# Performance work log

Hardware: AMD Instinct MI355X
Metric: run time of the kernel (lower is better)

## Reference

```python
import jax, jax.numpy as jnp
import numpy as np

C = 128  # out_channels per head for every layer
LAYERS = [(8, 4), (512, 2), (256, 1)]  # (in_dim, heads)
PARAM_NAMES = [f"{n}{l}" for l in (1, 2, 3)
               for n in ("Wl", "bl", "Wr", "br", "We", "att", "bo", "lnw", "lnb")]
N_NODES, N_EDGES, N_GRAPHS = 50000, 800000, 64


def _gatv2(x, src, dst, ea, Wl, bl, Wr, br, We, att, bo, H, N):
    # PyG GATv2Conv (share_weights=False, concat=True, negative_slope=0.2)
    xl = (x @ Wl + bl).reshape(N, H, C)          # lin_l -> source transform
    xr = (x @ Wr + br).reshape(N, H, C)          # lin_r -> dest transform
    ee = (ea @ We).reshape(-1, H, C)             # lin_edge (no bias)
    s = jax.nn.leaky_relu(xl[src] + xr[dst] + ee, 0.2)  # [E,H,C]
    logit = jnp.einsum('ehc,hc->eh', s, att)     # per-edge attention logits
    # segment softmax over incoming edges of each destination node
    m = jax.ops.segment_max(logit, dst, num_segments=N)
    a = jnp.exp(logit - m[dst])
    a = a / (jax.ops.segment_sum(a, dst, num_segments=N)[dst] + 1e-16)
    out = jax.ops.segment_sum(xl[src] * a[:, :, None], dst, num_segments=N)
    return out.reshape(N, H * C) + bo


def _graph_layernorm(x, w, b):
    # PyG LayerNorm(mode='graph') called without batch: normalize over ALL
    # nodes and features jointly, then per-feature affine.
    mu = x.mean()
    sd = x.std()
    return (x - mu) / (sd + 1e-5) * w + b


def _forward(x, edge_index, edge_attr, batch, params):
    N = x.shape[0]
    src, dst = edge_index[0], edge_index[1]
    # add_self_loops with fill_value='mean': self-loop edge_attr = mean of
    # attrs of edges entering that node (0 if none)
    cnt = jax.ops.segment_sum(jnp.ones((src.shape[0],), x.dtype), dst, num_segments=N)
    loop_attr = jax.ops.segment_sum(edge_attr, dst, num_segments=N) / jnp.maximum(cnt, 1.0)[:, None]
    ar = jnp.arange(N, dtype=src.dtype)
    src2 = jnp.concatenate([src, ar])
    dst2 = jnp.concatenate([dst, ar])
    ea2 = jnp.concatenate([edge_attr, loop_attr], axis=0)

    h = x
    for l, (_, H) in enumerate(LAYERS, 1):
        p = lambda n: params[f"{n}{l}"]
        h = _gatv2(h, src2, dst2, ea2, p("Wl"), p("bl"), p("Wr"), p("br"),
                   p("We"), p("att"), p("bo"), H, N)
        h = jax.nn.elu(_graph_layernorm(h, p("lnw"), p("lnb")))
        # dropout(0.25) is identity in eval mode

    # global mean pool || global max pool
    gcnt = jax.ops.segment_sum(jnp.ones((N,), h.dtype), batch, num_segments=N_GRAPHS)
    mean = jax.ops.segment_sum(h, batch, num_segments=N_GRAPHS) / jnp.maximum(gcnt, 1.0)[:, None]
    mx = jax.ops.segment_max(h, batch, num_segments=N_GRAPHS)
    mx = jnp.where(jnp.isfinite(mx), mx, 0.0)
    return jnp.concatenate([mean, mx], axis=1)  # [G, 256]


def setup_inputs() -> dict:
    key = jax.random.key(0)
    ks = iter(jax.random.split(key, 64))
    x = jax.random.normal(next(ks), (N_NODES, 8), jnp.float32)
    edge_index = jax.random.randint(next(ks), (2, N_EDGES), 0, N_NODES, dtype=jnp.int32)
    edge_attr = jax.random.normal(next(ks), (N_EDGES, 3), jnp.float32)
    batch = jnp.sort(jax.random.randint(next(ks), (N_NODES,), 0, N_GRAPHS, dtype=jnp.int32))

    def lin(k, i, o):
        return jax.random.normal(k, (i, o), jnp.float32) * np.float32(1.0 / np.sqrt(i))

    params = {}
    for l, (din, H) in enumerate(LAYERS, 1):
        params[f"Wl{l}"] = lin(next(ks), din, H * C)
        params[f"bl{l}"] = jnp.zeros((H * C,), jnp.float32)
        params[f"Wr{l}"] = lin(next(ks), din, H * C)
        params[f"br{l}"] = jnp.zeros((H * C,), jnp.float32)
        params[f"We{l}"] = lin(next(ks), 3, H * C)
        params[f"att{l}"] = jax.random.normal(next(ks), (H, C), jnp.float32) * np.float32(0.1)
        params[f"bo{l}"] = jnp.zeros((H * C,), jnp.float32)
        params[f"lnw{l}"] = jnp.ones((H * C,), jnp.float32)
        params[f"lnb{l}"] = jnp.zeros((H * C,), jnp.float32)
    return {"x": x, "edge_index": edge_index, "edge_attr": edge_attr, "batch": batch, **params}


def reference(x, edge_index, edge_attr, batch,
              Wl1, bl1, Wr1, br1, We1, att1, bo1, lnw1, lnb1,
              Wl2, bl2, Wr2, br2, We2, att2, bo2, lnw2, lnb2,
              Wl3, bl3, Wr3, br3, We3, att3, bo3, lnw3, lnb3):
    vals = [Wl1, bl1, Wr1, br1, We1, att1, bo1, lnw1, lnb1,
            Wl2, bl2, Wr2, br2, We2, att2, bo2, lnw2, lnb2,
            Wl3, bl3, Wr3, br3, We3, att3, bo3, lnw3, lnb3]
    return _forward(x, edge_index, edge_attr, batch, dict(zip(PARAM_NAMES, vals)))
```

## Files before the change

### kernel.cpp

```cpp
#include <hip/hip_runtime.h>
#include <hip/hip_bf16.h>
#include <math.h>

#define N_NODES 50000
#define N_EDGES 800000
#define N_GRAPHS 64
#define E2_TOTAL (N_EDGES + N_NODES)

typedef unsigned short u16;
typedef __attribute__((ext_vector_type(8))) short s16x8;
typedef __attribute__((ext_vector_type(4))) float f32x4;
typedef __attribute__((ext_vector_type(2))) float f32x2;

__device__ __forceinline__ u16 f2bf(float f) {
    unsigned u = __float_as_uint(f);
    u += 0x7fffu + ((u >> 16) & 1u);
    return (u16)(u >> 16);
}
__device__ __forceinline__ void unpack2(unsigned v, float& a, float& b) {
    a = __uint_as_float(v << 16);
    b = __uint_as_float(v & 0xffff0000u);
}
__device__ __forceinline__ f32x2 up2(unsigned v) {
    f32x2 r;
    r.x = __uint_as_float(v << 16);
    r.y = __uint_as_float(v & 0xffff0000u);
    return r;
}
__device__ __forceinline__ unsigned pack2(float a, float b) {
    return (unsigned)f2bf(a) | ((unsigned)f2bf(b) << 16);
}
__device__ __forceinline__ float elu_fast(float u) {
    return u > 0.f ? u : __expf(u) - 1.f;
}


__global__ __launch_bounds__(256) void deg_kernel(const int* __restrict__ ei,
                                                  const float* __restrict__ eattr,
                                                  int* __restrict__ deg,
                                                  float* __restrict__ asum, int E) {
    int e = blockIdx.x * 256 + threadIdx.x;
    if (e >= E) return;
    int dst = ei[E + e];
    atomicAdd(&deg[dst], 1);
    atomicAdd(&asum[dst * 3 + 0], eattr[e * 3 + 0]);
    atomicAdd(&asum[dst * 3 + 1], eattr[e * 3 + 1]);
    atomicAdd(&asum[dst * 3 + 2], eattr[e * 3 + 2]);
}

__global__ __launch_bounds__(1024) void scan_kernel(const int* __restrict__ deg,
                                                    int* __restrict__ rowptr,
                                                    int* __restrict__ cursor, int N) {
    __shared__ int wsum[16];
    __shared__ int carry_s;
    int tid = threadIdx.x, lane = tid & 63, wid = tid >> 6;
    if (tid == 0) carry_s = 0;
    __syncthreads();
    for (int base = 0; base < N; base += 4096) {
        int i0 = base + tid * 4;
        int d0 = (i0 + 0 < N) ? deg[i0 + 0] + 1 : 0;
        int d1 = (i0 + 1 < N) ? deg[i0 + 1] + 1 : 0;
        int d2 = (i0 + 2 < N) ? deg[i0 + 2] + 1 : 0;
        int d3 = (i0 + 3 < N) ? deg[i0 + 3] + 1 : 0;
        int v = d0 + d1 + d2 + d3;
        int x = v;
        #pragma unroll
        for (int off = 1; off < 64; off <<= 1) {
            int t = __shfl_up(x, off);
            if (lane >= off) x += t;
        }
        if (lane == 63) wsum[wid] = x;
        __syncthreads();
        if (wid == 0) {
            int y = (lane < 16) ? wsum[lane] : 0;
            #pragma unroll
            for (int off = 1; off < 16; off <<= 1) {
                int t = __shfl_up(y, off);
                if (lane >= off) y += t;
            }
            if (lane < 16) wsum[lane] = y;
        }
        __syncthreads();
        int woff = (wid > 0) ? wsum[wid - 1] : 0;
        int excl = carry_s + woff + x - v;
        if (i0 + 0 < N) { rowptr[i0 + 0] = excl;                cursor[i0 + 0] = excl; }
        if (i0 + 1 < N) { rowptr[i0 + 1] = excl + d0;           cursor[i0 + 1] = excl + d0; }
        if (i0 + 2 < N) { rowptr[i0 + 2] = excl + d0 + d1;      cursor[i0 + 2] = excl + d0 + d1; }
        if (i0 + 3 < N) { rowptr[i0 + 3] = excl + d0 + d1 + d2; cursor[i0 + 3] = excl + d0 + d1 + d2; }
        __syncthreads();
        if (tid == 1023) carry_s += wsum[15];
        __syncthreads();
    }
    if (threadIdx.x == 0) rowptr[N] = carry_s;
}

__global__ __launch_bounds__(256) void fill_kernel(const int* __restrict__ ei,
                                                   const float* __restrict__ eattr,
                                                   const float* __restrict__ asum,
                                                   const int* __restrict__ deg,
                                                   int* __restrict__ cursor,
                                                   float4* __restrict__ meta,
                                                   int E, int E2) {
    int e = blockIdx.x * 256 + threadIdx.x;
    if (e >= E2) return;
    int src, dst;
    float a0, a1, a2;
    if (e < E) {
        src = ei[e]; dst = ei[E + e];
        a0 = eattr[(size_t)e * 3 + 0];
        a1 = eattr[(size_t)e * 3 + 1];
        a2 = eattr[(size_t)e * 3 + 2];
    } else {
        src = e - E; dst = src;
        float inv = 1.0f / (float)max(deg[dst], 1);
        a0 = asum[(size_t)dst * 3 + 0] * inv;
        a1 = asum[(size_t)dst * 3 + 1] * inv;
        a2 = asum[(size_t)dst * 3 + 2] * inv;
    }
    int pos = atomicAdd(&cursor[dst], 1);
    meta[pos] = make_float4(a0, a1, a2, __int_as_float(src));
}


__global__ __launch_bounds__(256) void xw8_dual(const float* __restrict__ x,
                                                const float* __restrict__ Wl,
                                                const float* __restrict__ bl,
                                                const float* __restrict__ Wr,
                                                const float* __restrict__ br,
                                                u16* __restrict__ Xa,
                                                u16* __restrict__ Xb, int N) {
    __shared__ float sWl[8 * 512], sWr[8 * 512];
    __shared__ float sbl[512], sbr[512];
    __shared__ float sx[64][8];
    int tid = threadIdx.x;
    int nb = blockIdx.x * 64;
    for (int i = tid; i < 8 * 512; i += 256) { sWl[i] = Wl[i]; sWr[i] = Wr[i]; }
    for (int i = tid; i < 512; i += 256) { sbl[i] = bl[i]; sbr[i] = br[i]; }
    for (int i = tid; i < 64 * 8; i += 256) {
        int j = i >> 3, k = i & 7;
        int n = nb + j;
        sx[j][k] = (n < N) ? x[(size_t)n * 8 + k] : 0.f;
    }
    __syncthreads();
    for (int it = 0; it < 64; it++) {
        int i = tid + it * 256;
        int j = i >> 8, c2 = (i & 255) * 2;
        int n = nb + j;
        if (n < N) {
            float l0 = sbl[c2], l1 = sbl[c2 + 1];
            float r0 = sbr[c2], r1 = sbr[c2 + 1];
            #pragma unroll
            for (int k = 0; k < 8; k++) {
                float xv = sx[j][k];
                l0 += xv * sWl[k * 512 + c2];
                l1 += xv * sWl[k * 512 + c2 + 1];
                r0 += xv * sWr[k * 512 + c2];
                r1 += xv * sWr[k * 512 + c2 + 1];
            }
            *reinterpret_cast<unsigned*>(Xa + (size_t)n * 512 + c2) = pack2(l0, l1);
            *reinterpret_cast<unsigned*>(Xb + (size_t)n * 512 + c2) = pack2(r0, r1);
        }
    }
}


__device__ __forceinline__ float2 reduce_buckets(const double* __restrict__ buck,
                                                 double count) {
    __shared__ float2 res;
    int t = threadIdx.x;
    double s  = buck[t * 2]     + buck[(t + 256) * 2];
    double s2 = buck[t * 2 + 1] + buck[(t + 256) * 2 + 1];
    #pragma unroll
    for (int off = 32; off; off >>= 1) {
        s += __shfl_xor(s, off);
        s2 += __shfl_xor(s2, off);
    }
    __shared__ double a[4], b[4];
    int wid = t >> 6, lane = t & 63;
    if (lane == 0) { a[wid] = s; b[wid] = s2; }
    __syncthreads();
    if (t == 0) {
        double S = a[0] + a[1] + a[2] + a[3];
        double S2 = b[0] + b[1] + b[2] + b[3];
        double mu = S / count;
        double var = S2 / count - mu * mu;
        float sd = (float)sqrt(var > 0.0 ? var : 0.0);
        res.x = (float)mu;
        res.y = 1.f / (sd + 1e-5f);
    }
    __syncthreads();
    return res;
}


__global__ __launch_bounds__(256) void wt_dual(const float* __restrict__ WL,
                                               const float* __restrict__ WR,
                                               u16* __restrict__ WtL,
                                               u16* __restrict__ WtR, int K, int M) {
    const float* W = blockIdx.z ? WR : WL;
    u16* Wt = blockIdx.z ? WtR : WtL;
    __shared__ u16 t[64][65];
    int kb = blockIdx.x * 64, mb = blockIdx.y * 64;
    int tid = threadIdx.x;
    for (int i = tid; i < 64 * 64; i += 256) {
        int k = i >> 6, m = i & 63;
        t[m][k] = f2bf(W[(size_t)(kb + k) * M + mb + m]);
    }
    __syncthreads();
    for (int i = tid; i < 64 * 64; i += 256) {
        int m = i >> 6, k = i & 63;
        Wt[(size_t)(mb + m) * K + kb + k] = t[m][k];
    }
}


__global__ __launch_bounds__(256) void gemm_dual(const u16* __restrict__ A,
                                                 const u16* __restrict__ BtL,
                                                 const u16* __restrict__ BtR,
                                                 const float* __restrict__ biasL,
                                                 const float* __restrict__ biasR,
                                                 u16* __restrict__ YL,
                                                 u16* __restrict__ YR,
                                                 const double* __restrict__ buck,
                                                 double count,
                                                 const float* __restrict__ lnw,
                                                 const float* __restrict__ lnb,
                                                 int N, int K, int M) {
    const u16* Bt = blockIdx.z ? BtR : BtL;
    const float* bias = blockIdx.z ? biasR : biasL;
    u16* Y = blockIdx.z ? YR : YL;
    constexpr int BM = 128, BK = 64;
    __shared__ u16 As[BM][BK];
    __shared__ u16 Bs[BM][BK];
    __shared__ float sLw[512], sLb[512];
    float2 lp = reduce_buckets(buck, count);
    float muf = lp.x, rs = lp.y;
    int tid = threadIdx.x;
    for (int i = tid; i < K; i += 256) { sLw[i] = lnw[i] * rs; sLb[i] = lnb[i]; }
    int wid = tid >> 6, lane = tid & 63;
    int wm = (wid >> 1) * 64, wn = (wid & 1) * 64;
    int bm = blockIdx.x * BM, bn = blockIdx.y * BM;
    int l15 = lane & 15, l4 = lane >> 4;
    f32x4 acc[4][4] = {};
    int sr = tid >> 3;
    int cbw = tid & 7;
    int sc = cbw * 8;
    __syncthreads();

    for (int k0 = 0; k0 < K; k0 += BK) {
        #pragma unroll
        for (int p = 0; p < 4; p++) {
            int r = p * 32 + sr;
            int swc = ((cbw ^ (r & 7)) * 8);
            int grow = bm + r;
            uint4 av = make_uint4(0, 0, 0, 0);
            if (grow < N) {
                av = *reinterpret_cast<const uint4*>(A + (size_t)grow * K + k0 + sc);
                float f[8];
                unpack2(av.x, f[0], f[1]); unpack2(av.y, f[2], f[3]);
                unpack2(av.z, f[4], f[5]); unpack2(av.w, f[6], f[7]);
                #pragma unroll
                for (int q = 0; q < 8; q++) {
                    int c = k0 + sc + q;
                    f[q] = elu_fast((f[q] - muf) * sLw[c] + sLb[c]);
                }
                av = make_uint4(pack2(f[0], f[1]), pack2(f[2], f[3]),
                                pack2(f[4], f[5]), pack2(f[6], f[7]));
            }
            *reinterpret_cast<uint4*>(&As[r][swc]) = av;
            uint4 bv = *reinterpret_cast<const uint4*>(Bt + (size_t)(bn + r) * K + k0 + sc);
            *reinterpret_cast<uint4*>(&Bs[r][swc]) = bv;
        }
        __syncthreads();
        #pragma unroll
        for (int kk = 0; kk < 2; kk++) {
            int CB = kk * 4 + l4;
            s16x8 af[4], bfr[4];
            #pragma unroll
            for (int i = 0; i < 4; i++) {
                int Ra = wm + i * 16 + l15;
                int Rb = wn + i * 16 + l15;
                af[i]  = *reinterpret_cast<const s16x8*>(&As[Ra][(CB ^ (Ra & 7)) * 8]);
                bfr[i] = *reinterpret_cast<const s16x8*>(&Bs[Rb][(CB ^ (Rb & 7)) * 8]);
            }
            #pragma unroll
            for (int i = 0; i < 4; i++)
                #pragma unroll
                for (int j = 0; j < 4; j++)
                    acc[i][j] = __builtin_amdgcn_mfma_f32_16x16x32_bf16(
                        af[i], bfr[j], acc[i][j], 0, 0, 0);
        }
        __syncthreads();
    }
    #pragma unroll
    for (int i = 0; i < 4; i++) {
        #pragma unroll
        for (int j = 0; j < 4; j++) {
            int col = bn + wn + j * 16 + l15;
            float bv = bias[col];
            #pragma unroll
            for (int r = 0; r < 4; r++) {
                int row = bm + wm + i * 16 + l4 * 4 + r;
                if (row < N)
                    Y[(size_t)row * M + col] = f2bf(acc[i][j][r] + bv);
            }
        }
    }
}


template <int HC, int SPLIT, bool F32OUT>
__global__ __launch_bounds__(256) void attn_wave(
    const int* __restrict__ rowptr, const float4* __restrict__ meta,
    const u16* __restrict__ XLbf, const u16* __restrict__ XRbf,
    const float* __restrict__ We, const float* __restrict__ att,
    const float* __restrict__ bo, float* __restrict__ outf,
    u16* __restrict__ outb, double* __restrict__ sbuck, int N) {
    constexpr int CW  = HC / SPLIT;
    constexpr int CPL = CW / 64;
    constexpr int P2  = CPL / 2;
    constexpr int GS  = 128 / CPL;
    constexpr int SHB = (HC == 512) ? 10 : (HC == 256) ? 9 : 8;
    int gw = blockIdx.x * 4 + (threadIdx.x >> 6);
    int lane = threadIdx.x & 63;
    int n = gw / SPLIT;
    int sub = gw - n * SPLIT;
    if (n >= N) return;
    int cb = sub * CW + lane * CPL;

    f32x2 xr2[P2], we0v[P2], we1v[P2], we2v[P2], sav[P2], accv[P2];
    #pragma unroll
    for (int i = 0; i < P2; i++) {
        we0v[i] = *reinterpret_cast<const f32x2*>(&We[cb + 2 * i]);
        we1v[i] = *reinterpret_cast<const f32x2*>(&We[HC + cb + 2 * i]);
        we2v[i] = *reinterpret_cast<const f32x2*>(&We[2 * HC + cb + 2 * i]);
        sav[i]  = *reinterpret_cast<const f32x2*>(&att[cb + 2 * i]);
        accv[i] = f32x2{0.f, 0.f};
    }
    auto ldrow = [&](const u16* base, int idx) -> uint4 {
        const u16* p = (const u16*)((const char*)base +
                       ((size_t)((unsigned)idx << SHB))) + cb;
        if constexpr (CPL == 8) {
            return *reinterpret_cast<const uint4*>(p);
        } else if constexpr (CPL == 4) {
            uint2 r = *reinterpret_cast<const uint2*>(p);
            return make_uint4(r.x, r.y, 0, 0);
        } else {
            return make_uint4(*reinterpret_cast<const unsigned*>(p), 0, 0, 0);
        }
    };
    auto toF2 = [&](uint4 r, f32x2* v) {
        v[0] = up2(r.x);
        if constexpr (CPL >= 4) v[1] = up2(r.y);
        if constexpr (CPL == 8) { v[2] = up2(r.z); v[3] = up2(r.w); }
    };
    {
        uint4 r = ldrow(XRbf, n);
        toF2(r, xr2);
    }

    int beg = __builtin_amdgcn_readfirstlane(rowptr[n]);
    int end = __builtin_amdgcn_readfirstlane(rowptr[n + 1]);
    int e1 = end - 1;
    float m = -INFINITY, l = 0.f;

    float4 mdA = meta[beg];
    float4 mdB = meta[min(beg + 1, e1)];
    int sA = __builtin_amdgcn_readfirstlane(__float_as_int(mdA.w));
    int sB = __builtin_amdgcn_readfirstlane(__float_as_int(mdB.w));
    uint4 rA = ldrow(XLbf, sA), rB = ldrow(XLbf, sB);

    for (int j = beg; j < end; j += 2) {
        float4 mdA_n = meta[min(j + 2, e1)];
        float4 mdB_n = meta[min(j + 3, e1)];
        int sAn = __builtin_amdgcn_readfirstlane(__float_as_int(mdA_n.w));
        int sBn = __builtin_amdgcn_readfirstlane(__float_as_int(mdB_n.w));
        uint4 rA_n = ldrow(XLbf, sAn), rB_n = ldrow(XLbf, sBn);

        f32x2 xl0v[P2], xl1v[P2];
        toF2(rA, xl0v);
        toF2(rB, xl1v);
        f32x2 pv0 = {0.f, 0.f}, pv1 = {0.f, 0.f};
        f32x2 ax0 = {mdA.x, mdA.x}, ay0 = {mdA.y, mdA.y}, az0 = {mdA.z, mdA.z};
        f32x2 ax1 = {mdB.x, mdB.x}, ay1 = {mdB.y, mdB.y}, az1 = {mdB.z, mdB.z};
        #pragma unroll
        for (int i = 0; i < P2; i++) {
            f32x2 u0 = __builtin_elementwise_fma(ax0, we0v[i],
                       __builtin_elementwise_fma(ay0, we1v[i],
                       __builtin_elementwise_fma(az0, we2v[i], xl0v[i] + xr2[i])));
            f32x2 u1 = __builtin_elementwise_fma(ax1, we0v[i],
                       __builtin_elementwise_fma(ay1, we1v[i],
                       __builtin_elementwise_fma(az1, we2v[i], xl1v[i] + xr2[i])));
            f32x2 lr0 = __builtin_elementwise_max(u0, u0 * 0.2f);
            f32x2 lr1 = __builtin_elementwise_max(u1, u1 * 0.2f);
            pv0 = __builtin_elementwise_fma(lr0, sav[i], pv0);
            pv1 = __builtin_elementwise_fma(lr1, sav[i], pv1);
        }
        float p0 = pv0.x + pv0.y;
        float p1 = pv1.x + pv1.y;
        #pragma unroll
        for (int off = GS / 2; off >= 1; off >>= 1) {
            p0 += __shfl_xor(p0, off);
            p1 += __shfl_xor(p1, off);
        }
        if (j + 1 > e1) p1 = -INFINITY;
        float hi = fmaxf(p0, p1);
        if (__all(hi <= m + 8.f)) {
            float w0 = __expf(p0 - m), w1 = __expf(p1 - m);
            l += w0 + w1;
            f32x2 w0v = {w0, w0}, w1v = {w1, w1};
            #pragma unroll
            for (int i = 0; i < P2; i++)
                accv[i] = __builtin_elementwise_fma(w0v, xl0v[i],
                          __builtin_elementwise_fma(w1v, xl1v[i], accv[i]));
        } else {
            float mn = fmaxf(m, hi);
            float sc = __expf(m - mn);
            float w0 = __expf(p0 - mn), w1 = __expf(p1 - mn);
            l = fmaf(l, sc, w0 + w1);
            f32x2 scv = {sc, sc}, w0v = {w0, w0}, w1v = {w1, w1};
            #pragma unroll
            for (int i = 0; i < P2; i++)
                accv[i] = __builtin_elementwise_fma(accv[i], scv,
                          __builtin_elementwise_fma(w0v, xl0v[i], w1v * xl1v[i]));
            m = mn;
        }
        mdA = mdA_n; mdB = mdB_n; rA = rA_n; rB = rB_n;
    }

    float inv = 1.f / (l + 1e-16f);
    f32x2 invv = {inv, inv};
    f32x2 ov[P2];
    float s = 0.f, s2 = 0.f;
    #pragma unroll
    for (int i = 0; i < P2; i++) {
        f32x2 bov = *reinterpret_cast<const f32x2*>(&bo[cb + 2 * i]);
        ov[i] = __builtin_elementwise_fma(accv[i], invv, bov);
        s += ov[i].x + ov[i].y;
        s2 += ov[i].x * ov[i].x + ov[i].y * ov[i].y;
    }
    if constexpr (F32OUT) {
        float* q = outf + (size_t)n * HC + cb;
        if constexpr (CPL == 8) {
            *reinterpret_cast<float4*>(q)     = make_float4(ov[0].x, ov[0].y, ov[1].x, ov[1].y);
            *reinterpret_cast<float4*>(q + 4) = make_float4(ov[2].x, ov[2].y, ov[3].x, ov[3].y);
        } else if constexpr (CPL == 4) {
            *reinterpret_cast<float4*>(q) = make_float4(ov[0].x, ov[0].y, ov[1].x, ov[1].y);
        } else {
            *reinterpret_cast<float2*>(q) = make_float2(ov[0].x, ov[0].y);
        }
    } else {
        u16* q = outb + (size_t)n * HC + cb;
        if constexpr (CPL == 8) {
            *reinterpret_cast<uint4*>(q) =
                make_uint4(pack2(ov[0].x, ov[0].y), pack2(ov[1].x, ov[1].y),
                           pack2(ov[2].x, ov[2].y), pack2(ov[3].x, ov[3].y));
        } else if constexpr (CPL == 4) {
            *reinterpret_cast<uint2*>(q) =
                make_uint2(pack2(ov[0].x, ov[0].y), pack2(ov[1].x, ov[1].y));
        } else {
            *reinterpret_cast<unsigned*>(q) = pack2(ov[0].x, ov[0].y);
        }
    }
    #pragma unroll
    for (int off = 32; off; off >>= 1) {
        s += __shfl_xor(s, off);
        s2 += __shfl_xor(s2, off);
    }
    if (lane == 0) {
        double* bk = sbuck + (size_t)(blockIdx.x & 511) * 2;
        atomicAdd(bk, (double)s);
        atomicAdd(bk + 1, (double)s2);
    }
}


__global__ __launch_bounds__(256) void pool_ln(const float* __restrict__ h,
                                               const int* __restrict__ batch,
                                               const double* __restrict__ buck,
                                               double count,
                                               const float* __restrict__ lw,
                                               const float* __restrict__ lb,
                                               float* __restrict__ out, int N) {
    float2 lp = reduce_buckets(buck, count);
    __shared__ float sh[128], mh[128];
    int g = blockIdx.x;
    int s_ = 0, hi_ = N;
    while (s_ < hi_) { int mid = (s_ + hi_) >> 1; if (batch[mid] < g) s_ = mid + 1; else hi_ = mid; }
    int e_ = s_, hi2 = N;
    while (e_ < hi2) { int mid = (e_ + hi2) >> 1; if (batch[mid] < g + 1) e_ = mid + 1; else hi2 = mid; }
    int tid = threadIdx.x;
    int c = tid & 127, part = tid >> 7;
    float wc = lw[c] * lp.y, bc = lb[c];
    float sum = 0.f, mx = -INFINITY;
    for (int n = s_ + part; n < e_; n += 2) {
        float v = elu_fast((h[(size_t)n * 128 + c] - lp.x) * wc + bc);
        sum += v;
        mx = fmaxf(mx, v);
    }
    if (part == 1) { sh[c] = sum; mh[c] = mx; }
    __syncthreads();
    if (part == 0) {
        if (e_ - s_ > 1) { sum += sh[c]; mx = fmaxf(mx, mh[c]); }
        int cnt = e_ - s_;
        out[g * 256 + c] = cnt > 0 ? sum / (float)cnt : 0.f;
        out[g * 256 + 128 + c] = cnt > 0 ? mx : 0.f;
    }
}


extern "C" void kernel_launch(void* const* d_in, const int* in_sizes, int n_in,
                              void* d_out, int out_size, void* d_ws, size_t ws_size,
                              hipStream_t stream) {
    const int N = N_NODES, E = N_EDGES, G = N_GRAPHS, E2 = E2_TOTAL;
    const float* x = (const float*)d_in[0];
    const int* ei = (const int*)d_in[1];
    const float* eattr = (const float*)d_in[2];
    const int* batch = (const int*)d_in[3];
    auto P = [&](int l, int k) { return (const float*)d_in[4 + l * 9 + k]; };

    char* w = (char*)d_ws;
    size_t off = 0;
    auto alloc = [&](size_t bytes) -> void* {
        void* p = w + off;
        off += (bytes + 255) & ~(size_t)255;
        return p;
    };
    u16* Xa = (u16*)alloc((size_t)N * 512 * 2);
    u16* Xb = (u16*)alloc((size_t)N * 512 * 2);
    u16* Xc = (u16*)alloc((size_t)N * 512 * 2);
    float* H3f = (float*)alloc((size_t)N * 128 * 4);
    float4* meta = (float4*)alloc((size_t)E2 * 16);
    u16* WtL = (u16*)alloc((size_t)512 * 256 * 2);
    u16* WtR = (u16*)alloc((size_t)512 * 256 * 2);
    int* rowptr = (int*)alloc((size_t)(N + 1) * 4);
    int* cursor = (int*)alloc((size_t)N * 4);
    size_t zs = off;
    int* deg = (int*)alloc((size_t)N * 4);
    float* asum = (float*)alloc((size_t)N * 3 * 4);
    double* b1 = (double*)alloc(512 * 2 * 8);
    double* b2 = (double*)alloc(512 * 2 * 8);
    double* b3 = (double*)alloc(512 * 2 * 8);
    size_t ze = off;
    (void)ws_size; (void)n_in; (void)in_sizes; (void)out_size;

    hipMemsetAsync(w + zs, 0, ze - zs, stream);

    deg_kernel<<<(E + 255) / 256, 256, 0, stream>>>(ei, eattr, deg, asum, E);
    scan_kernel<<<1, 1024, 0, stream>>>(deg, rowptr, cursor, N);
    fill_kernel<<<(E2 + 255) / 256, 256, 0, stream>>>(ei, eattr, asum, deg, cursor,
                                                      meta, E, E2);

    xw8_dual<<<(N + 63) / 64, 256, 0, stream>>>(x, P(0, 0), P(0, 1), P(0, 2), P(0, 3),
                                                Xa, Xb, N);
    attn_wave<512, 1, false><<<(N + 3) / 4, 256, 0, stream>>>(
        rowptr, meta, Xa, Xb, P(0, 4), P(0, 5), P(0, 6), nullptr, Xc, b1, N);

    {
        dim3 tg(512 / 64, 256 / 64, 2);
        wt_dual<<<tg, 256, 0, stream>>>(P(1, 0), P(1, 2), WtL, WtR, 512, 256);
        dim3 gg((N + 127) / 128, 2, 2);
        gemm_dual<<<gg, 256, 0, stream>>>(Xc, WtL, WtR, P(1, 1), P(1, 3),
                                          Xa, Xb, b1, (double)N * 512.0,
                                          P(0, 7), P(0, 8), N, 512, 256);
    }
    attn_wave<256, 1, false><<<(N + 3) / 4, 256, 0, stream>>>(
        rowptr, meta, Xa, Xb, P(1, 4), P(1, 5), P(1, 6), nullptr, Xc, b2, N);

    {
        dim3 tg(256 / 64, 128 / 64, 2);
        wt_dual<<<tg, 256, 0, stream>>>(P(2, 0), P(2, 2), WtL, WtR, 256, 128);
        dim3 gg((N + 127) / 128, 1, 2);
        gemm_dual<<<gg, 256, 0, stream>>>(Xc, WtL, WtR, P(2, 1), P(2, 3),
                                          Xa, Xb, b2, (double)N * 256.0,
                                          P(1, 7), P(1, 8), N, 256, 128);
    }
    attn_wave<128, 1, true><<<(N + 3) / 4, 256, 0, stream>>>(
        rowptr, meta, Xa, Xb, P(2, 4), P(2, 5), P(2, 6), H3f, nullptr, b3, N);

    pool_ln<<<G, 256, 0, stream>>>(H3f, batch, b3, (double)N * 128.0,
                                   P(2, 7), P(2, 8), (float*)d_out, N);
}
```

Measured before the change: 869.0 us.

## Fuse degree counting with layer-1 projection and merge L/R GEMMs sharing A tile

Merges the edge degree/attr-sum kernel and the layer-1 input projection into one launch by giving each its own range of block indices. The dual GEMM now computes both the left and right projections in one block, loading and layer-normalizing the A tile once instead of twice. This removes one launch and halves the A-side loads and normalization work. In exchange it doubles the accumulator registers per thread and adds another LDS buffer, which may lower occupancy. It also halves the GEMM grid, leaving fewer blocks to spread across the CUs.

```diff
diff --git a/kernel.cpp b/kernel.cpp
--- a/kernel.cpp
+++ b/kernel.cpp
@@ -6,6 +6,8 @@
 #define N_EDGES 800000
 #define N_GRAPHS 64
 #define E2_TOTAL (N_EDGES + N_NODES)
+#define NBX ((N_NODES + 63) / 64)
+#define NBD ((N_EDGES + 255) / 256)
 
 typedef unsigned short u16;
 typedef __attribute__((ext_vector_type(8))) short s16x8;
@@ -35,17 +37,55 @@
 }
 
 
-__global__ __launch_bounds__(256) void deg_kernel(const int* __restrict__ ei,
-                                                  const float* __restrict__ eattr,
-                                                  int* __restrict__ deg,
-                                                  float* __restrict__ asum, int E) {
-    int e = blockIdx.x * 256 + threadIdx.x;
-    if (e >= E) return;
-    int dst = ei[E + e];
-    atomicAdd(&deg[dst], 1);
-    atomicAdd(&asum[dst * 3 + 0], eattr[e * 3 + 0]);
-    atomicAdd(&asum[dst * 3 + 1], eattr[e * 3 + 1]);
-    atomicAdd(&asum[dst * 3 + 2], eattr[e * 3 + 2]);
+__global__ __launch_bounds__(256) void prep_kernel(
+    const float* __restrict__ x, const float* __restrict__ Wl,
+    const float* __restrict__ bl, const float* __restrict__ Wr,
+    const float* __restrict__ br, u16* __restrict__ Xa, u16* __restrict__ Xb,
+    const int* __restrict__ ei, const float* __restrict__ eattr,
+    int* __restrict__ deg, float* __restrict__ asum, int N, int E) {
+    int tid = threadIdx.x;
+    if (blockIdx.x >= NBX) {
+        int e = (blockIdx.x - NBX) * 256 + tid;
+        if (e < E) {
+            int dst = ei[E + e];
+            atomicAdd(&deg[dst], 1);
+            atomicAdd(&asum[dst * 3 + 0], eattr[e * 3 + 0]);
+            atomicAdd(&asum[dst * 3 + 1], eattr[e * 3 + 1]);
+            atomicAdd(&asum[dst * 3 + 2], eattr[e * 3 + 2]);
+        }
+        return;
+    }
+    __shared__ float sWl[8 * 512], sWr[8 * 512];
+    __shared__ float sbl[512], sbr[512];
+    __shared__ float sx[64][8];
+    int nb = blockIdx.x * 64;
+    for (int i = tid; i < 8 * 512; i += 256) { sWl[i] = Wl[i]; sWr[i] = Wr[i]; }
+    for (int i = tid; i < 512; i += 256) { sbl[i] = bl[i]; sbr[i] = br[i]; }
+    for (int i = tid; i < 64 * 8; i += 256) {
+        int j = i >> 3, k = i & 7;
+        int n = nb + j;
+        sx[j][k] = (n < N) ? x[(size_t)n * 8 + k] : 0.f;
+    }
+    __syncthreads();
+    for (int it = 0; it < 64; it++) {
+        int i = tid + it * 256;
+        int j = i >> 8, c2 = (i & 255) * 2;
+        int n = nb + j;
+        if (n < N) {
+            float l0 = sbl[c2], l1 = sbl[c2 + 1];
+            float r0 = sbr[c2], r1 = sbr[c2 + 1];
+            #pragma unroll
+            for (int k = 0; k < 8; k++) {
+                float xv = sx[j][k];
+                l0 += xv * sWl[k * 512 + c2];
+                l1 += xv * sWl[k * 512 + c2 + 1];
+                r0 += xv * sWr[k * 512 + c2];
+                r1 += xv * sWr[k * 512 + c2 + 1];
+            }
+            *reinterpret_cast<unsigned*>(Xa + (size_t)n * 512 + c2) = pack2(l0, l1);
+            *reinterpret_cast<unsigned*>(Xb + (size_t)n * 512 + c2) = pack2(r0, r1);
+        }
+    }
 }
 
 __global__ __launch_bounds__(1024) void scan_kernel(const int* __restrict__ deg,
@@ -122,48 +162,6 @@
 }
 
 
-__global__ __launch_bounds__(256) void xw8_dual(const float* __restrict__ x,
-                                                const float* __restrict__ Wl,
-                                                const float* __restrict__ bl,
-                                                const float* __restrict__ Wr,
-                                                const float* __restrict__ br,
-                                                u16* __restrict__ Xa,
-                                                u16* __restrict__ Xb, int N) {
-    __shared__ float sWl[8 * 512], sWr[8 * 512];
-    __shared__ float sbl[512], sbr[512];
-    __shared__ float sx[64][8];
-    int tid = threadIdx.x;
-    int nb = blockIdx.x * 64;
-    for (int i = tid; i < 8 * 512; i += 256) { sWl[i] = Wl[i]; sWr[i] = Wr[i]; }
-    for (int i = tid; i < 512; i += 256) { sbl[i] = bl[i]; sbr[i] = br[i]; }
-    for (int i = tid; i < 64 * 8; i += 256) {
-        int j = i >> 3, k = i & 7;
-        int n = nb + j;
-        sx[j][k] = (n < N) ? x[(size_t)n * 8 + k] : 0.f;
-    }
-    __syncthreads();
-    for (int it = 0; it < 64; it++) {
-        int i = tid + it * 256;
-        int j = i >> 8, c2 = (i & 255) * 2;
-        int n = nb + j;
-        if (n < N) {
-            float l0 = sbl[c2], l1 = sbl[c2 + 1];
-            float r0 = sbr[c2], r1 = sbr[c2 + 1];
-            #pragma unroll
-            for (int k = 0; k < 8; k++) {
-                float xv = sx[j][k];
-                l0 += xv * sWl[k * 512 + c2];
-                l1 += xv * sWl[k * 512 + c2 + 1];
-                r0 += xv * sWr[k * 512 + c2];
-                r1 += xv * sWr[k * 512 + c2 + 1];
-            }
-            *reinterpret_cast<unsigned*>(Xa + (size_t)n * 512 + c2) = pack2(l0, l1);
-            *reinterpret_cast<unsigned*>(Xb + (size_t)n * 512 + c2) = pack2(r0, r1);
-        }
-    }
-}
-
-
 __device__ __forceinline__ float2 reduce_buckets(const double* __restrict__ buck,
                                                  double count) {
     __shared__ float2 res;
@@ -214,24 +212,22 @@
 }
 
 
-__global__ __launch_bounds__(256) void gemm_dual(const u16* __restrict__ A,
-                                                 const u16* __restrict__ BtL,
-                                                 const u16* __restrict__ BtR,
-                                                 const float* __restrict__ biasL,
-                                                 const float* __restrict__ biasR,
-                                                 u16* __restrict__ YL,
-                                                 u16* __restrict__ YR,
-                                                 const double* __restrict__ buck,
-                                                 double count,
-                                                 const float* __restrict__ lnw,
-                                                 const float* __restrict__ lnb,
-                                                 int N, int K, int M) {
-    const u16* Bt = blockIdx.z ? BtR : BtL;
-    const float* bias = blockIdx.z ? biasR : biasL;
-    u16* Y = blockIdx.z ? YR : YL;
+__global__ __launch_bounds__(256) void gemm_LR(const u16* __restrict__ A,
+                                               const u16* __restrict__ BtL,
+                                               const u16* __restrict__ BtR,
+                                               const float* __restrict__ biasL,
+                                               const float* __restrict__ biasR,
+                                               u16* __restrict__ YL,
+                                               u16* __restrict__ YR,
+                                               const double* __restrict__ buck,
+                                               double count,
+                                               const float* __restrict__ lnw,
+                                               const float* __restrict__ lnb,
+                                               int N, int K, int M) {
     constexpr int BM = 128, BK = 64;
     __shared__ u16 As[BM][BK];
-    __shared__ u16 Bs[BM][BK];
+    __shared__ u16 BsL[BM][BK];
+    __shared__ u16 BsR[BM][BK];
     __shared__ float sLw[512], sLb[512];
     float2 lp = reduce_buckets(buck, count);
     float muf = lp.x, rs = lp.y;
@@ -241,7 +237,8 @@
     int wm = (wid >> 1) * 64, wn = (wid & 1) * 64;
     int bm = blockIdx.x * BM, bn = blockIdx.y * BM;
     int l15 = lane & 15, l4 = lane >> 4;
-    f32x4 acc[4][4] = {};
+    f32x4 accL[4][4] = {};
+    f32x4 accR[4][4] = {};
     int sr = tid >> 3;
     int cbw = tid & 7;
     int sc = cbw * 8;
@@ -268,27 +265,35 @@
                                 pack2(f[4], f[5]), pack2(f[6], f[7]));
             }
             *reinterpret_cast<uint4*>(&As[r][swc]) = av;
-            uint4 bv = *reinterpret_cast<const uint4*>(Bt + (size_t)(bn + r) * K + k0 + sc);
-            *reinterpret_cast<uint4*>(&Bs[r][swc]) = bv;
+            *reinterpret_cast<uint4*>(&BsL[r][swc]) =
+                *reinterpret_cast<const uint4*>(BtL + (size_t)(bn + r) * K + k0 + sc);
+            *reinterpret_cast<uint4*>(&BsR[r][swc]) =
+                *reinterpret_cast<const uint4*>(BtR + (size_t)(bn + r) * K + k0 + sc);
         }
         __syncthreads();
         #pragma unroll
         for (int kk = 0; kk < 2; kk++) {
             int CB = kk * 4 + l4;
-            s16x8 af[4], bfr[4];
+            s16x8 af[4], bfL[4], bfR[4];
             #pragma unroll
             for (int i = 0; i < 4; i++) {
                 int Ra = wm + i * 16 + l15;
                 int Rb = wn + i * 16 + l15;
-                af[i]  = *reinterpret_cast<const s16x8*>(&As[Ra][(CB ^ (Ra & 7)) * 8]);
-                bfr[i] = *reinterpret_cast<const s16x8*>(&Bs[Rb][(CB ^ (Rb & 7)) * 8]);
+                int sa = (CB ^ (Ra & 7)) * 8;
+                int sb = (CB ^ (Rb & 7)) * 8;
+                af[i]  = *reinterpret_cast<const s16x8*>(&As[Ra][sa]);
+                bfL[i] = *reinterpret_cast<const s16x8*>(&BsL[Rb][sb]);
+                bfR[i] = *reinterpret_cast<const s16x8*>(&BsR[Rb][sb]);
             }
             #pragma unroll
             for (int i = 0; i < 4; i++)
                 #pragma unroll
-                for (int j = 0; j < 4; j++)
-                    acc[i][j] = __builtin_amdgcn_mfma_f32_16x16x32_bf16(
-                        af[i], bfr[j], acc[i][j], 0, 0, 0);
+                for (int j = 0; j < 4; j++) {
+                    accL[i][j] = __builtin_amdgcn_mfma_f32_16x16x32_bf16(
+                        af[i], bfL[j], accL[i][j], 0, 0, 0);
+                    accR[i][j] = __builtin_amdgcn_mfma_f32_16x16x32_bf16(
+                        af[i], bfR[j], accR[i][j], 0, 0, 0);
+                }
         }
         __syncthreads();
     }
@@ -297,12 +302,15 @@
         #pragma unroll
         for (int j = 0; j < 4; j++) {
             int col = bn + wn + j * 16 + l15;
-            float bv = bias[col];
+            float bvL = biasL[col];
+            float bvR = biasR[col];
             #pragma unroll
             for (int r = 0; r < 4; r++) {
                 int row = bm + wm + i * 16 + l4 * 4 + r;
-                if (row < N)
-                    Y[(size_t)row * M + col] = f2bf(acc[i][j][r] + bv);
+                if (row < N) {
+                    YL[(size_t)row * M + col] = f2bf(accL[i][j][r] + bvL);
+                    YR[(size_t)row * M + col] = f2bf(accR[i][j][r] + bvR);
+                }
             }
         }
     }
@@ -546,23 +554,22 @@
 
     hipMemsetAsync(w + zs, 0, ze - zs, stream);
 
-    deg_kernel<<<(E + 255) / 256, 256, 0, stream>>>(ei, eattr, deg, asum, E);
+    prep_kernel<<<NBX + NBD, 256, 0, stream>>>(x, P(0, 0), P(0, 1), P(0, 2), P(0, 3),
+                                               Xa, Xb, ei, eattr, deg, asum, N, E);
     scan_kernel<<<1, 1024, 0, stream>>>(deg, rowptr, cursor, N);
     fill_kernel<<<(E2 + 255) / 256, 256, 0, stream>>>(ei, eattr, asum, deg, cursor,
                                                       meta, E, E2);
 
-    xw8_dual<<<(N + 63) / 64, 256, 0, stream>>>(x, P(0, 0), P(0, 1), P(0, 2), P(0, 3),
-                                                Xa, Xb, N);
     attn_wave<512, 1, false><<<(N + 3) / 4, 256, 0, stream>>>(
         rowptr, meta, Xa, Xb, P(0, 4), P(0, 5), P(0, 6), nullptr, Xc, b1, N);
 
     {
         dim3 tg(512 / 64, 256 / 64, 2);
         wt_dual<<<tg, 256, 0, stream>>>(P(1, 0), P(1, 2), WtL, WtR, 512, 256);
-        dim3 gg((N + 127) / 128, 2, 2);
-        gemm_dual<<<gg, 256, 0, stream>>>(Xc, WtL, WtR, P(1, 1), P(1, 3),
-                                          Xa, Xb, b1, (double)N * 512.0,
-                                          P(0, 7), P(0, 8), N, 512, 256);
+        dim3 gg((N + 127) / 128, 2);
+        gemm_LR<<<gg, 256, 0, stream>>>(Xc, WtL, WtR, P(1, 1), P(1, 3),
+                                        Xa, Xb, b1, (double)N * 512.0,
+                                        P(0, 7), P(0, 8), N, 512, 256);
     }
     attn_wave<256, 1, false><<<(N + 3) / 4, 256, 0, stream>>>(
         rowptr, meta, Xa, Xb, P(1, 4), P(1, 5), P(1, 6), nullptr, Xc, b2, N);
@@ -570,10 +577,10 @@
     {
         dim3 tg(256 / 64, 128 / 64, 2);
         wt_dual<<<tg, 256, 0, stream>>>(P(2, 0), P(2, 2), WtL, WtR, 256, 128);
-        dim3 gg((N + 127) / 128, 1, 2);
-        gemm_dual<<<gg, 256, 0, stream>>>(Xc, WtL, WtR, P(2, 1), P(2, 3),
-                                          Xa, Xb, b2, (double)N * 256.0,
-                                          P(1, 7), P(1, 8), N, 256, 128);
+        dim3 gg((N + 127) / 128, 1);
+        gemm_LR<<<gg, 256, 0, stream>>>(Xc, WtL, WtR, P(2, 1), P(2, 3),
+                                        Xa, Xb, b2, (double)N * 256.0,
+                                        P(1, 7), P(1, 8), N, 256, 128);
     }
     attn_wave<128, 1, true><<<(N + 3) / 4, 256, 0, stream>>>(
         rowptr, meta, Xa, Xb, P(2, 4), P(2, 5), P(2, 6), H3f, nullptr, b3, N);
```

Result: no change. 860.4 us (-1.0%).
